# Optimization experiments

Measured on AMD Instinct MI355X. Metric: run time of the kernel, lower is better.

The kernel has to match this reference:

```python
import jax, jax.numpy as jnp
import numpy as np
from jax import lax

NUM_GROUPS = 16
POOL_K = 2
CLAMP_MIN = 0.0
CLAMP_MAX = 1.0
EPS = 1e-5


def setup_inputs() -> dict:
    key = jax.random.key(0)
    k1, k2, k3, k4, k5, k6 = jax.random.split(key, 6)
    B, Cin, H, W = 32, 64, 128, 128
    Cout, K = 128, 3
    x = jax.random.normal(k1, (B, Cin, H, W), dtype=jnp.float32)
    conv_w = jax.random.normal(k2, (Cout, Cin, K, K), dtype=jnp.float32) * 0.05
    conv_b = jax.random.normal(k3, (Cout,), dtype=jnp.float32) * 0.05
    gn_weight = jnp.ones((Cout,), dtype=jnp.float32) + 0.1 * jax.random.normal(k4, (Cout,), dtype=jnp.float32)
    gn_bias = 0.1 * jax.random.normal(k5, (Cout,), dtype=jnp.float32)
    scale = jnp.ones((Cout, 1, 1), dtype=jnp.float32) + 0.1 * jax.random.normal(k6, (Cout, 1, 1), dtype=jnp.float32)
    return {"x": x, "conv_w": conv_w, "conv_b": conv_b,
            "gn_weight": gn_weight, "gn_bias": gn_bias, "scale": scale}


def reference(x, conv_w, conv_b, gn_weight, gn_bias, scale):
    # Conv2d, VALID padding, stride 1  -> [B, C, H-2, W-2]
    y = lax.conv_general_dilated(
        x, conv_w, window_strides=(1, 1), padding='VALID',
        dimension_numbers=('NCHW', 'OIHW', 'NCHW'))
    y = y + conv_b[None, :, None, None]

    B, C, H, W = y.shape
    # GroupNorm: stats per (batch, group) over channels_per_group*H*W
    yg = y.reshape(B, NUM_GROUPS, -1)
    mean = jnp.mean(yg, axis=-1, keepdims=True)
    var = jnp.mean(jnp.square(yg - mean), axis=-1, keepdims=True)
    yn = ((yg - mean) * lax.rsqrt(var + EPS)).reshape(B, C, H, W)
    # affine + extra per-channel scale (fused elementwise)
    yn = (yn * gn_weight[None, :, None, None] + gn_bias[None, :, None, None]) * scale[None]

    # MaxPool2d(k=POOL_K), VALID, stride=k
    p = lax.reduce_window(yn, -jnp.inf, lax.max,
                          (1, 1, POOL_K, POOL_K), (1, 1, POOL_K, POOL_K), 'VALID')
    return jnp.clip(p, CLAMP_MIN, CLAMP_MAX)
```

## Files before the change

kernel.cpp:

```cpp
#include <hip/hip_runtime.h>

typedef _Float16 half8 __attribute__((ext_vector_type(8)));
typedef _Float16 half4t __attribute__((ext_vector_type(4)));
typedef _Float16 half2t __attribute__((ext_vector_type(2)));
typedef float float4t __attribute__((ext_vector_type(4)));
typedef float float4u __attribute__((ext_vector_type(4), aligned(4)));

#define BATCH 32
#define CIN 64
#define HIN 128
#define WIN 128
#define COUT 128
#define HOUT 126
#define WOUT 126
#define YSTR 128
#define HP 63
#define WP 63
#define NGROUPS 16
#define CPG 8
#define EPSV 1e-5f

#define XP_ROW 8320

__global__ __launch_bounds__(256) void wt_kernel(const float* __restrict__ w,
                                                 _Float16* __restrict__ wT) {
    int idx = blockIdx.x * 256 + threadIdx.x;
    if (idx >= 9 * COUT * CIN) return;
    int cin = idx & 63;
    int t = idx >> 6;
    int cout = t & 127;
    int pos = t >> 7;
    wT[idx] = (_Float16)w[(cout * CIN + cin) * 9 + pos];
}

__global__ __launch_bounds__(256) void repack_kernel(const float* __restrict__ x,
                                                     _Float16* __restrict__ xp) {
    __shared__ _Float16 lt[128 * 66];
    const int tid = threadIdx.x;
    const int grow = blockIdx.x;
    const int b = blockIdx.y;

    const int c0 = tid >> 5;
    const int col0 = (tid & 31) * 4;
#pragma unroll
    for (int i = 0; i < 8; i++) {
        int cin = c0 + 8 * i;
        float4t v = *(const float4t*)(x + (((size_t)b * CIN + cin) * HIN + grow) * WIN + col0);
#pragma unroll
        for (int j = 0; j < 4; j++)
            lt[(col0 + j) * 66 + cin] = (_Float16)v[j];
    }
    __syncthreads();

    _Float16* xpb = xp + ((size_t)b * HIN + grow) * XP_ROW;
#pragma unroll
    for (int k = 0; k < 4; k++) {
        int cidx = tid + 256 * k;
        int col = cidx >> 3, chk = cidx & 7;
        half8 v = *(const half8*)&lt[col * 66 + chk * 8];
        int slot = chk ^ ((2 * grow + col) & 7);
        *(half8*)(xpb + col * 64 + slot * 8) = v;
    }
    if (tid < 16) {
        int col = 128 + (tid >> 3), chk = tid & 7;
        int slot = chk ^ ((2 * grow + col) & 7);
        half8 z;
#pragma unroll
        for (int j = 0; j < 8; j++) z[j] = (_Float16)0.f;
        *(half8*)(xpb + col * 64 + slot * 8) = z;
    }
}

__global__ __launch_bounds__(256, 3) void conv_mfma_kernel(
    const _Float16* __restrict__ xp, const _Float16* __restrict__ wT,
    const float* __restrict__ bias, _Float16* __restrict__ yh,
    float* __restrict__ stats)
{
    __shared__ __align__(16) _Float16 xs[25088];

    const int tid = threadIdx.x;
    int f = blockIdx.y * 126 + blockIdx.x;
    int w = (f & 7) * 504 + (f >> 3);
    const int oy = w % 126;
    const int b  = w / 126;

    const int lane = tid & 63;
    const int wv   = tid >> 6;

    {
        const char* src = (const char*)(xp + (size_t)(b * HIN + oy) * XP_ROW);
        const int wb = wv * 1024;
#pragma unroll
        for (int k = 0; k < 12; k++) {
            __builtin_amdgcn_global_load_lds(
                (const __attribute__((address_space(1))) void*)(src + k * 4096 + wb + lane * 16),
                (__attribute__((address_space(3))) void*)((char*)xs + k * 4096 + wb),
                16, 0, 0);
        }
        if (wv == 0) {
            __builtin_amdgcn_global_load_lds(
                (const __attribute__((address_space(1))) void*)(src + 49152 + lane * 16),
                (__attribute__((address_space(3))) void*)((char*)xs + 49152),
                16, 0, 0);
        }
    }
    __syncthreads();

    const int m    = lane & 15;
    const int q    = lane >> 4;
    const int cout0 = (tid >> 6) * 32;

    float4t acc[2][8];
#pragma unroll
    for (int s = 0; s < 2; s++)
#pragma unroll
        for (int n = 0; n < 8; n++)
            acc[s][n] = (float4t){0.f, 0.f, 0.f, 0.f};

    const _Float16* ab0 = wT + (size_t)(cout0 + m) * CIN + q * 8;
    half8 a0 = *(const half8*)(ab0);
    half8 a1 = *(const half8*)(ab0 + 16 * CIN);

    for (int kk = 0; kk < 18; kk++) {
        int pos = kk >> 1, ch = kk & 1;
        int kh = (pos > 2) + (pos > 5);
        int kw = pos - kh * 3;
        int key = (2 * (oy + kh) + m + kw) & 7;
        const _Float16* bb = &xs[(kh * 130 + m + kw) * 64 + (((q + 4 * ch) ^ key) << 3)];

        half8 na0 = a0, na1 = a1;
        if (kk < 17) {
            int nk = kk + 1, npos = nk >> 1, nch = nk & 1;
            const _Float16* ab = wT + ((size_t)(npos * COUT + cout0 + m)) * CIN + q * 8 + nch * 32;
            na0 = *(const half8*)ab;
            na1 = *(const half8*)(ab + 16 * CIN);
        }
#pragma unroll
        for (int n = 0; n < 8; n++) {
            half8 bf = *(const half8*)(bb + n * 1024);
            acc[0][n] = __builtin_amdgcn_mfma_f32_16x16x32_f16(bf, a0, acc[0][n], 0, 0, 0);
            acc[1][n] = __builtin_amdgcn_mfma_f32_16x16x32_f16(bf, a1, acc[1][n], 0, 0, 0);
        }
        a0 = na0; a1 = na1;
    }

#pragma unroll
    for (int sub = 0; sub < 2; sub++) {
        const int c = cout0 + sub * 16 + m;
        const float bv = bias[c];
        _Float16* yrow = yh + (((size_t)b * COUT + c) * HOUT + oy) * YSTR;
        float sv = 0.f, ssv = 0.f;
#pragma unroll
        for (int n = 0; n < 8; n++) {
            int pix0 = n * 16 + q * 4;
            float v0 = acc[sub][n][0] + bv;
            float v1 = acc[sub][n][1] + bv;
            float v2 = acc[sub][n][2] + bv;
            float v3 = acc[sub][n][3] + bv;
            sv  += v0 + v1;
            ssv += v0 * v0 + v1 * v1;
            if (pix0 + 3 < WOUT) {
                sv  += v2 + v3;
                ssv += v2 * v2 + v3 * v3;
            }
            half4t hv = { (_Float16)v0, (_Float16)v1, (_Float16)v2, (_Float16)v3 };
            *(half4t*)(yrow + pix0) = hv;
        }
        sv  += __shfl_xor(sv, 1);   ssv += __shfl_xor(ssv, 1);
        sv  += __shfl_xor(sv, 2);   ssv += __shfl_xor(ssv, 2);
        sv  += __shfl_xor(sv, 4);   ssv += __shfl_xor(ssv, 4);
        sv  += __shfl_xor(sv, 16);  ssv += __shfl_xor(ssv, 16);
        sv  += __shfl_xor(sv, 32);  ssv += __shfl_xor(ssv, 32);
        if ((lane & 55) == 0) {
            int g = (cout0 >> 3) + sub * 2 + ((lane >> 3) & 1);
            atomicAdd(&stats[(b * NGROUPS + g) * 2 + 0], sv);
            atomicAdd(&stats[(b * NGROUPS + g) * 2 + 1], ssv);
        }
    }
}

__global__ __launch_bounds__(256) void norm_pool_kernel(
    const _Float16* __restrict__ yh, const float* __restrict__ stats,
    const float* __restrict__ gnw, const float* __restrict__ gnb,
    const float* __restrict__ scale, float* __restrict__ out)
{
    const int t  = threadIdx.x & 15;
    const int hs = threadIdx.x >> 4;
    const int hblk = blockIdx.x & 3;
    const int c = (blockIdx.x >> 2) & 127;
    const int b = blockIdx.x >> 9;
    const int hp = hblk * 16 + hs;

    const float N = (float)(CPG * HOUT * WOUT);
    int g = c >> 3;
    float sum   = stats[(b * NGROUPS + g) * 2 + 0];
    float sumsq = stats[(b * NGROUPS + g) * 2 + 1];
    float mean = sum / N;
    float var  = sumsq / N - mean * mean;
    float rstd = rsqrtf(var + EPSV);

    float gw = gnw[c] * rstd;
    float A  = gw * scale[c];
    float B2 = (gnb[c] - mean * gw) * scale[c];

    if (hp >= HP) return;

    const _Float16* yp = yh + ((((size_t)b * COUT + c) * HOUT + hp * 2) << 7) + t * 8;
    half8 r0 = *(const half8*)yp;
    half8 r1 = *(const half8*)(yp + YSTR);

    float o[4];
#pragma unroll
    for (int j = 0; j < 4; j++) {
        float v0 = fmaf((float)r0[2 * j],     A, B2);
        float v1 = fmaf((float)r0[2 * j + 1], A, B2);
        float v2 = fmaf((float)r1[2 * j],     A, B2);
        float v3 = fmaf((float)r1[2 * j + 1], A, B2);
        float mx = fmaxf(fmaxf(v0, v1), fmaxf(v2, v3));
        o[j] = fminf(fmaxf(mx, 0.0f), 1.0f);
    }

    float* op = out + (((size_t)b * COUT + c) * HP + hp) * WP + t * 4;
    if (t < 15) {
        *(float4u*)op = (float4u){o[0], o[1], o[2], o[3]};
    } else {
        op[0] = o[0]; op[1] = o[1]; op[2] = o[2];
    }
}

extern "C" void kernel_launch(void* const* d_in, const int* in_sizes, int n_in,
                              void* d_out, int out_size, void* d_ws, size_t ws_size,
                              hipStream_t stream) {
    const float* x      = (const float*)d_in[0];
    const float* conv_w = (const float*)d_in[1];
    const float* conv_b = (const float*)d_in[2];
    const float* gnw    = (const float*)d_in[3];
    const float* gnb    = (const float*)d_in[4];
    const float* scale  = (const float*)d_in[5];
    float* out = (float*)d_out;

    const size_t y_bytes = (size_t)BATCH * COUT * HOUT * YSTR * sizeof(_Float16);
    _Float16* yh = (_Float16*)d_ws;
    float* stats = (float*)((char*)d_ws + y_bytes);
    _Float16* wT = (_Float16*)((char*)d_ws + y_bytes + 4096);
    _Float16* xp = (_Float16*)((char*)d_ws + y_bytes + 4096 + 147456);

    hipMemsetAsync(stats, 0, BATCH * NGROUPS * 2 * sizeof(float), stream);

    wt_kernel<<<(9 * COUT * CIN + 255) / 256, 256, 0, stream>>>(conv_w, wT);

    dim3 rgrid(HIN, BATCH);
    repack_kernel<<<rgrid, 256, 0, stream>>>(x, xp);

    dim3 grid(HOUT, BATCH);
    conv_mfma_kernel<<<grid, 256, 0, stream>>>(xp, wT, conv_b, yh, stats);

    norm_pool_kernel<<<BATCH * COUT * 4, 256, 0, stream>>>(
        yh, stats, gnw, gnb, scale, out);
}
```

Measured before the change: 385.1 us.

## Process conv row strips with rolling LDS buffer and fuse 2x2 pooling pre-reduction

```diff
diff --git a/kernel.cpp b/kernel.cpp
--- a/kernel.cpp
+++ b/kernel.cpp
@@ -13,14 +13,15 @@
 #define COUT 128
 #define HOUT 126
 #define WOUT 126
-#define YSTR 128
 #define HP 63
 #define WP 63
 #define NGROUPS 16
 #define CPG 8
 #define EPSV 1e-5f
 
-#define XP_ROW 8320
+#define XPR 8320
+#define XPRB 16640
+#define STRIP 6
 
 __global__ __launch_bounds__(256) void wt_kernel(const float* __restrict__ w,
                                                  _Float16* __restrict__ wT) {
@@ -40,26 +41,30 @@
     const int grow = blockIdx.x;
     const int b = blockIdx.y;
 
-    const int c0 = tid >> 5;
+    const int u = tid >> 5;
     const int col0 = (tid & 31) * 4;
-#pragma unroll
-    for (int i = 0; i < 8; i++) {
-        int cin = c0 + 8 * i;
-        float4t v = *(const float4t*)(x + (((size_t)b * CIN + cin) * HIN + grow) * WIN + col0);
-#pragma unroll
-        for (int j = 0; j < 4; j++)
-            lt[(col0 + j) * 66 + cin] = (_Float16)v[j];
+    const float* xb = x + ((size_t)b * CIN * HIN + grow) * WIN;
+#pragma unroll
+    for (int i = 0; i < 4; i++) {
+        int cin0 = 2 * (u + 8 * i);
+        float4t va = *(const float4t*)(xb + (size_t)cin0 * HIN * WIN + col0);
+        float4t vb = *(const float4t*)(xb + (size_t)(cin0 + 1) * HIN * WIN + col0);
+#pragma unroll
+        for (int j = 0; j < 4; j++) {
+            half2t hv = { (_Float16)va[j], (_Float16)vb[j] };
+            *(half2t*)&lt[(col0 + j) * 66 + cin0] = hv;
+        }
     }
     __syncthreads();
 
-    _Float16* xpb = xp + ((size_t)b * HIN + grow) * XP_ROW;
-#pragma unroll
-    for (int k = 0; k < 4; k++) {
+    _Float16* xpb = xp + ((size_t)b * HIN + grow) * XPR;
+#pragma unroll
+    for (int k = 0; k < 16; k++) {
         int cidx = tid + 256 * k;
-        int col = cidx >> 3, chk = cidx & 7;
-        half8 v = *(const half8*)&lt[col * 66 + chk * 8];
-        int slot = chk ^ ((2 * grow + col) & 7);
-        *(half8*)(xpb + col * 64 + slot * 8) = v;
+        int col = cidx >> 5, p = cidx & 31;
+        half2t v = *(const half2t*)&lt[col * 66 + 2 * p];
+        int slot = (p >> 2) ^ ((2 * grow + col) & 7);
+        *(half2t*)(xpb + col * 64 + slot * 8 + (p & 3) * 2) = v;
     }
     if (tid < 16) {
         int col = 128 + (tid >> 3), chk = tid & 7;
@@ -71,116 +76,147 @@
     }
 }
 
-__global__ __launch_bounds__(256, 3) void conv_mfma_kernel(
+__global__ __launch_bounds__(256, 2) void conv_mfma_kernel(
     const _Float16* __restrict__ xp, const _Float16* __restrict__ wT,
-    const float* __restrict__ bias, _Float16* __restrict__ yh,
+    const float* __restrict__ bias, unsigned int* __restrict__ pl,
     float* __restrict__ stats)
 {
-    __shared__ __align__(16) _Float16 xs[25088];
+    __shared__ __align__(16) _Float16 xs[4 * XPR];
 
     const int tid = threadIdx.x;
-    int f = blockIdx.y * 126 + blockIdx.x;
-    int w = (f & 7) * 504 + (f >> 3);
-    const int oy = w % 126;
-    const int b  = w / 126;
+    const int s = blockIdx.x;
+    const int b = blockIdx.y;
+    const int R0 = STRIP * s;
 
     const int lane = tid & 63;
-    const int wv   = tid >> 6;
-
-    {
-        const char* src = (const char*)(xp + (size_t)(b * HIN + oy) * XP_ROW);
-        const int wb = wv * 1024;
-#pragma unroll
-        for (int k = 0; k < 12; k++) {
+    const int wv = tid >> 6;
+    const int w2 = wv & 1;
+    const int nh = wv >> 1;
+    const int m = lane & 15;
+    const int q = lane >> 4;
+    const int cb = w2 * 64;
+
+    auto stage = [&](int r) {
+        const char* src = (const char*)(xp + ((size_t)b * HIN + r) * XPR);
+        char* dst = (char*)xs + (r & 3) * XPRB;
+#pragma unroll
+        for (int k = 0; k < 4; k++) {
+            int off = (wv * 4 + k) * 1024;
             __builtin_amdgcn_global_load_lds(
-                (const __attribute__((address_space(1))) void*)(src + k * 4096 + wb + lane * 16),
-                (__attribute__((address_space(3))) void*)((char*)xs + k * 4096 + wb),
-                16, 0, 0);
+                (const __attribute__((address_space(1))) void*)(src + off + lane * 16),
+                (__attribute__((address_space(3))) void*)(dst + off), 16, 0, 0);
         }
         if (wv == 0) {
             __builtin_amdgcn_global_load_lds(
-                (const __attribute__((address_space(1))) void*)(src + 49152 + lane * 16),
-                (__attribute__((address_space(3))) void*)((char*)xs + 49152),
-                16, 0, 0);
-        }
-    }
+                (const __attribute__((address_space(1))) void*)(src + 16384 + lane * 4),
+                (__attribute__((address_space(3))) void*)(dst + 16384), 4, 0, 0);
+        }
+    };
+
+    stage(R0); stage(R0 + 1); stage(R0 + 2);
+
+    half8 a[4], na[4];
+#pragma unroll
+    for (int sub = 0; sub < 4; sub++)
+        a[sub] = *(const half8*)(wT + ((size_t)(cb + sub * 16 + m)) * CIN + q * 8);
+
+    float bv[4];
+#pragma unroll
+    for (int sub = 0; sub < 4; sub++) bv[sub] = bias[cb + sub * 16 + m];
+
+    float sv[4] = {0.f, 0.f, 0.f, 0.f}, ssv[4] = {0.f, 0.f, 0.f, 0.f};
+    half4t prow[4][4];
+
     __syncthreads();
 
-    const int m    = lane & 15;
-    const int q    = lane >> 4;
-    const int cout0 = (tid >> 6) * 32;
-
-    float4t acc[2][8];
-#pragma unroll
-    for (int s = 0; s < 2; s++)
-#pragma unroll
-        for (int n = 0; n < 8; n++)
-            acc[s][n] = (float4t){0.f, 0.f, 0.f, 0.f};
-
-    const _Float16* ab0 = wT + (size_t)(cout0 + m) * CIN + q * 8;
-    half8 a0 = *(const half8*)(ab0);
-    half8 a1 = *(const half8*)(ab0 + 16 * CIN);
-
-    for (int kk = 0; kk < 18; kk++) {
-        int pos = kk >> 1, ch = kk & 1;
-        int kh = (pos > 2) + (pos > 5);
-        int kw = pos - kh * 3;
-        int key = (2 * (oy + kh) + m + kw) & 7;
-        const _Float16* bb = &xs[(kh * 130 + m + kw) * 64 + (((q + 4 * ch) ^ key) << 3)];
-
-        half8 na0 = a0, na1 = a1;
-        if (kk < 17) {
-            int nk = kk + 1, npos = nk >> 1, nch = nk & 1;
-            const _Float16* ab = wT + ((size_t)(npos * COUT + cout0 + m)) * CIN + q * 8 + nch * 32;
-            na0 = *(const half8*)ab;
-            na1 = *(const half8*)(ab + 16 * CIN);
-        }
-#pragma unroll
-        for (int n = 0; n < 8; n++) {
-            half8 bf = *(const half8*)(bb + n * 1024);
-            acc[0][n] = __builtin_amdgcn_mfma_f32_16x16x32_f16(bf, a0, acc[0][n], 0, 0, 0);
-            acc[1][n] = __builtin_amdgcn_mfma_f32_16x16x32_f16(bf, a1, acc[1][n], 0, 0, 0);
-        }
-        a0 = na0; a1 = na1;
-    }
-
-#pragma unroll
-    for (int sub = 0; sub < 2; sub++) {
-        const int c = cout0 + sub * 16 + m;
-        const float bv = bias[c];
-        _Float16* yrow = yh + (((size_t)b * COUT + c) * HOUT + oy) * YSTR;
-        float sv = 0.f, ssv = 0.f;
-#pragma unroll
-        for (int n = 0; n < 8; n++) {
-            int pix0 = n * 16 + q * 4;
-            float v0 = acc[sub][n][0] + bv;
-            float v1 = acc[sub][n][1] + bv;
-            float v2 = acc[sub][n][2] + bv;
-            float v3 = acc[sub][n][3] + bv;
-            sv  += v0 + v1;
-            ssv += v0 * v0 + v1 * v1;
-            if (pix0 + 3 < WOUT) {
-                sv  += v2 + v3;
-                ssv += v2 * v2 + v3 * v3;
+    for (int i = 0; i < STRIP; i++) {
+        const int r = R0 + i;
+        if (i < STRIP - 1) stage(r + 3);
+
+        float4t acc[4][4];
+#pragma unroll
+        for (int sub = 0; sub < 4; sub++)
+#pragma unroll
+            for (int n = 0; n < 4; n++)
+                acc[sub][n] = (float4t){0.f, 0.f, 0.f, 0.f};
+
+        for (int kk = 0; kk < 18; kk++) {
+            int pos = kk >> 1, ch = kk & 1;
+            int kh = (pos > 2) + (pos > 5);
+            int kw = pos - kh * 3;
+            int rr = r + kh;
+            int key = (2 * rr + m + kw) & 7;
+            const _Float16* bb = &xs[(rr & 3) * XPR + (m + kw) * 64 + (((q + 4 * ch) ^ key) << 3)];
+
+            int nk = (kk == 17) ? 0 : kk + 1;
+            int npos = nk >> 1, nch = nk & 1;
+#pragma unroll
+            for (int sub = 0; sub < 4; sub++)
+                na[sub] = *(const half8*)(wT + ((size_t)(npos * COUT + cb + sub * 16 + m)) * CIN + q * 8 + nch * 32);
+
+#pragma unroll
+            for (int n = 0; n < 4; n++) {
+                half8 bf = *(const half8*)(bb + (nh * 4 + n) * 1024);
+#pragma unroll
+                for (int sub = 0; sub < 4; sub++)
+                    acc[sub][n] = __builtin_amdgcn_mfma_f32_16x16x32_f16(bf, a[sub], acc[sub][n], 0, 0, 0);
             }
-            half4t hv = { (_Float16)v0, (_Float16)v1, (_Float16)v2, (_Float16)v3 };
-            *(half4t*)(yrow + pix0) = hv;
-        }
-        sv  += __shfl_xor(sv, 1);   ssv += __shfl_xor(ssv, 1);
-        sv  += __shfl_xor(sv, 2);   ssv += __shfl_xor(ssv, 2);
-        sv  += __shfl_xor(sv, 4);   ssv += __shfl_xor(ssv, 4);
-        sv  += __shfl_xor(sv, 16);  ssv += __shfl_xor(ssv, 16);
-        sv  += __shfl_xor(sv, 32);  ssv += __shfl_xor(ssv, 32);
+#pragma unroll
+            for (int sub = 0; sub < 4; sub++) a[sub] = na[sub];
+        }
+
+        const bool odd = (i & 1) != 0;
+#pragma unroll
+        for (int sub = 0; sub < 4; sub++) {
+#pragma unroll
+            for (int n = 0; n < 4; n++) {
+                int pix0 = (nh * 4 + n) * 16 + q * 4;
+                float v0 = acc[sub][n][0] + bv[sub];
+                float v1 = acc[sub][n][1] + bv[sub];
+                float v2 = acc[sub][n][2] + bv[sub];
+                float v3 = acc[sub][n][3] + bv[sub];
+                sv[sub] += v0 + v1;
+                ssv[sub] += v0 * v0 + v1 * v1;
+                if (pix0 != 124) {
+                    sv[sub] += v2 + v3;
+                    ssv[sub] += v2 * v2 + v3 * v3;
+                }
+                _Float16 x0 = (_Float16)fmaxf(v0, v1), n0 = (_Float16)fminf(v0, v1);
+                _Float16 x1 = (_Float16)fmaxf(v2, v3), n1 = (_Float16)fminf(v2, v3);
+                if (!odd) {
+                    prow[sub][n] = (half4t){x0, n0, x1, n1};
+                } else {
+                    half4t p = prow[sub][n];
+                    half4t o = { p[0] > x0 ? p[0] : x0, p[1] < n0 ? p[1] : n0,
+                                 p[2] > x1 ? p[2] : x1, p[3] < n1 ? p[3] : n1 };
+                    int c = cb + sub * 16 + m;
+                    unsigned int* dst = pl + (((size_t)b * COUT + c) * HP + (r >> 1)) * 64
+                                        + (nh * 4 + n) * 8 + 2 * q;
+                    *(half4t*)dst = o;
+                }
+            }
+        }
+        __syncthreads();
+    }
+
+#pragma unroll
+    for (int sub = 0; sub < 4; sub++) {
+        float aa = sv[sub], cc = ssv[sub];
+        aa += __shfl_xor(aa, 1);  cc += __shfl_xor(cc, 1);
+        aa += __shfl_xor(aa, 2);  cc += __shfl_xor(cc, 2);
+        aa += __shfl_xor(aa, 4);  cc += __shfl_xor(cc, 4);
+        aa += __shfl_xor(aa, 16); cc += __shfl_xor(cc, 16);
+        aa += __shfl_xor(aa, 32); cc += __shfl_xor(cc, 32);
         if ((lane & 55) == 0) {
-            int g = (cout0 >> 3) + sub * 2 + ((lane >> 3) & 1);
-            atomicAdd(&stats[(b * NGROUPS + g) * 2 + 0], sv);
-            atomicAdd(&stats[(b * NGROUPS + g) * 2 + 1], ssv);
+            int g = w2 * 8 + sub * 2 + ((lane >> 3) & 1);
+            atomicAdd(&stats[(b * NGROUPS + g) * 2 + 0], aa);
+            atomicAdd(&stats[(b * NGROUPS + g) * 2 + 1], cc);
         }
     }
 }
 
 __global__ __launch_bounds__(256) void norm_pool_kernel(
-    const _Float16* __restrict__ yh, const float* __restrict__ stats,
+    const unsigned int* __restrict__ pl, const float* __restrict__ stats,
     const float* __restrict__ gnw, const float* __restrict__ gnb,
     const float* __restrict__ scale, float* __restrict__ out)
 {
@@ -205,18 +241,15 @@
 
     if (hp >= HP) return;
 
-    const _Float16* yp = yh + ((((size_t)b * COUT + c) * HOUT + hp * 2) << 7) + t * 8;
-    half8 r0 = *(const half8*)yp;
-    half8 r1 = *(const half8*)(yp + YSTR);
+    const unsigned int* yp = pl + (((size_t)b * COUT + c) * HP + hp) * 64 + t * 4;
+    half8 rv = *(const half8*)yp;
 
     float o[4];
 #pragma unroll
     for (int j = 0; j < 4; j++) {
-        float v0 = fmaf((float)r0[2 * j],     A, B2);
-        float v1 = fmaf((float)r0[2 * j + 1], A, B2);
-        float v2 = fmaf((float)r1[2 * j],     A, B2);
-        float v3 = fmaf((float)r1[2 * j + 1], A, B2);
-        float mx = fmaxf(fmaxf(v0, v1), fmaxf(v2, v3));
+        float vx = fmaf((float)rv[2 * j],     A, B2);
+        float vn = fmaf((float)rv[2 * j + 1], A, B2);
+        float mx = fmaxf(vx, vn);
         o[j] = fminf(fmaxf(mx, 0.0f), 1.0f);
     }
 
@@ -239,11 +272,11 @@
     const float* scale  = (const float*)d_in[5];
     float* out = (float*)d_out;
 
-    const size_t y_bytes = (size_t)BATCH * COUT * HOUT * YSTR * sizeof(_Float16);
-    _Float16* yh = (_Float16*)d_ws;
-    float* stats = (float*)((char*)d_ws + y_bytes);
-    _Float16* wT = (_Float16*)((char*)d_ws + y_bytes + 4096);
-    _Float16* xp = (_Float16*)((char*)d_ws + y_bytes + 4096 + 147456);
+    const size_t pl_bytes = (size_t)BATCH * COUT * HP * 64 * 4;
+    unsigned int* pl = (unsigned int*)d_ws;
+    float* stats = (float*)((char*)d_ws + pl_bytes);
+    _Float16* wT = (_Float16*)((char*)d_ws + pl_bytes + 4096);
+    _Float16* xp = (_Float16*)((char*)d_ws + pl_bytes + 4096 + 147456);
 
     hipMemsetAsync(stats, 0, BATCH * NGROUPS * 2 * sizeof(float), stream);
 
@@ -252,9 +285,9 @@
     dim3 rgrid(HIN, BATCH);
     repack_kernel<<<rgrid, 256, 0, stream>>>(x, xp);
 
-    dim3 grid(HOUT, BATCH);
-    conv_mfma_kernel<<<grid, 256, 0, stream>>>(xp, wT, conv_b, yh, stats);
+    dim3 grid(HOUT / STRIP, BATCH);
+    conv_mfma_kernel<<<grid, 256, 0, stream>>>(xp, wT, conv_b, pl, stats);
 
     norm_pool_kernel<<<BATCH * COUT * 4, 256, 0, stream>>>(
-        yh, stats, gnw, gnb, scale, out);
-}
+        pl, stats, gnw, gnb, scale, out);
+}
```

Result: slower. 433.3 us (+12.5%).
